# Kernel optimization log

Measured on AMD Instinct MI355X. Metric: run time of the kernel, lower is better.

Reference implementation:

```python
import jax, jax.numpy as jnp
import numpy as np

BIT_WIDTH = 1
LEVELS = 2 ** BIT_WIDTH - 1
# Floyd-Steinberg gather weights (mirrored scatter kernel): contributions to
# pixel (r,c) from (r-1,c-1), (r-1,c), (r-1,c+1), (r,c-1)
W_UL, W_U, W_UR, W_L = 1.0 / 16, 5.0 / 16, 3.0 / 16, 7.0 / 16


def quant(x):
    return jnp.round(x * LEVELS) / LEVELS


def dither(x01):
    """Raster-scan error-diffusion dithering. x01: [B,C,R,W] in [0,1]."""
    B, C, R, W = x01.shape
    dtype = x01.dtype

    def row_step(prev_err, row_x):
        # prev_err: [B,C,W+2] zero-padded errors of previous row
        # row_x:    [W,B,C]   input values of current row
        up = (W_UL * prev_err[..., 0:W]
              + W_U * prev_err[..., 1:W + 1]
              + W_UR * prev_err[..., 2:W + 2])          # [B,C,W]
        up = jnp.moveaxis(up, -1, 0)                     # [W,B,C]

        def col_step(left_err, xs):
            x, u = xs                                    # each [B,C]
            val = jnp.clip(x + u + W_L * left_err, 0.0, 1.0)
            err = val - quant(val)
            return err, (val, err)

        _, (vals, errs) = jax.lax.scan(col_step, jnp.zeros((B, C), dtype), (row_x, up))
        err_row = jnp.pad(jnp.moveaxis(errs, 0, -1), ((0, 0), (0, 0), (1, 1)))  # [B,C,W+2]
        return err_row, jnp.moveaxis(vals, 0, -1)        # carry, [B,C,W]

    rows_x = jnp.moveaxis(jnp.moveaxis(x01, 2, 0), -1, 1)  # [R,W,B,C]
    init = jnp.zeros((B, C, W + 2), dtype)
    _, out_rows = jax.lax.scan(row_step, init, rows_x)      # [R,B,C,W]
    out = jnp.moveaxis(out_rows, 0, 2)                      # [B,C,R,W]
    return quant(out)


def setup_inputs() -> dict:
    key = jax.random.key(0)
    x = jax.random.normal(key, (32, 3, 512, 512), dtype=jnp.float32)
    return {"x": x}


def reference(x):
    x = jnp.clip(x, -1.0, 1.0)
    x01 = (x + 1.0) / 2.0
    y = dither(x01)
    return y * 2.0 - 1.0
```

## Files before the change

### kernel.cpp

```cpp
#include <hip/hip_runtime.h>


#define F_UL 0.0625f
#define F_U  0.3125f
#define F_UR 0.1875f
#define F_L  0.4375f

constexpr int WW    = 512;
constexpr int IMG   = WW * WW;
constexpr int NIMG  = 96;
constexpr int NW    = 8;
constexpr int BUFW  = 792;
constexpr int NCH   = 40;
constexpr int LAG   = 10;
constexpr int PPAIR = 320;
constexpr size_t XP_FLOATS = (size_t)NIMG * NW * PPAIR * 128;
constexpr size_t XP_BYTES  = XP_FLOATS * 4;
constexpr size_t XP_SLACK  = 8192;
constexpr size_t XP_OFF    = 4u * 1024 * 1024;
constexpr size_t WS_NEED   = XP_OFF + XP_BYTES + XP_SLACK;

__device__ __forceinline__ float wave_shr1(float v, float fill) {
  int r = __builtin_amdgcn_update_dpp(__float_as_int(fill), __float_as_int(v),
                                      0x138 , 0xF, 0xF, false);
  return __int_as_float(r);
}

__device__ __forceinline__ float pp(float xv) {
#pragma clang fp contract(off)
  float xc = fminf(fmaxf(xv, -1.0f), 1.0f);
  return (xc + 1.0f) * 0.5f;
}

__global__ __launch_bounds__(256)
void pack_kernel(const float* __restrict__ xin, float* __restrict__ xp) {
  __shared__ float ring[4 * 4160];
  const int img = blockIdx.x, w = blockIdx.y;
  const int tid = threadIdx.x;
  const int wv  = tid >> 6, l = tid & 63;

  const float* xg = xin + (size_t)img * IMG + (size_t)w * 64 * WW;
  float* ob = xp + ((size_t)(img * NW + w) * PPAIR) * 128;

  auto load_tile = [&](int t) {
    float* dst = ring + (t & 3) * 4160;
    const float* src = xg + 64 * t;
#pragma unroll
    for (int k = 0; k < 4; ++k) {
      int flat = tid + 256 * k;
      int row = flat >> 4, cq = flat & 15;
      float4 v = *(const float4*)(src + row * WW + cq * 4);
      float* d = dst + row * 65 + cq * 4;
      d[0] = pp(v.x); d[1] = pp(v.y); d[2] = pp(v.z); d[3] = pp(v.w);
    }
  };

  load_tile(0);
  __syncthreads();
  for (int t = 0; t < 10; ++t) {
    if (t < 7) load_tile(t + 1);
    const int Mb = 32 * t + 8 * wv;
#pragma unroll
    for (int i = 0; i < 8; ++i) {
      const int M  = Mb + i;
      const int g  = 2 * (M - l);
      const int gm = g & 511;
      const int idx = ((gm >> 6) & 3) * 4160 + l * 65 + (gm & 63);
      const bool ok = ((unsigned)g < 512u);
      float va = ring[idx], vb = ring[idx + 1];
      float2 v = make_float2(ok ? va : -8.0f, ok ? vb : -8.0f);
      *(float2*)(ob + (size_t)M * 128 + 2 * l) = v;
    }
    __syncthreads();
  }
}

__global__ __launch_bounds__(512, 1)
void dither_packed(const float* __restrict__ xp, uint2* __restrict__ yb) {
  __shared__ float bnd[(NW + 1) * BUFW];
  __shared__ int flags[NW];

  const int  tid  = threadIdx.x;
  const int  wave = tid >> 6;
  const int  lane = tid & 63;
  const int  img  = blockIdx.x;
  const bool l63  = (lane == 63);

  for (int i = tid; i < (NW + 1) * BUFW; i += 512) bnd[i] = 0.0f;
  if (tid < NW) flags[tid] = 0;
  __syncthreads();

  uint2* ybw = yb + (size_t)(img * NW + wave) * (10 * 64);
  const float* xw = xp + ((size_t)(img * NW + wave) * PPAIR) * 128 + lane * 2;
  float* bufR = bnd + wave * BUFW;
  float* bufW = bnd + (wave + 1) * BUFW;

  float2 X0[4], X1[4], X2[4], X3[4], X4[4], X5[4], X6[4], X7[4];
#pragma unroll
  for (int i = 0; i < 4; ++i) {
    X0[i] = *(const float2*)(xw + (size_t)(0  + i) * 128);
    X1[i] = *(const float2*)(xw + (size_t)(4  + i) * 128);
    X2[i] = *(const float2*)(xw + (size_t)(8  + i) * 128);
    X3[i] = *(const float2*)(xw + (size_t)(12 + i) * 128);
  }

  int seen = 0;
  if (wave) {
    while ((seen = __hip_atomic_load(&flags[wave - 1], __ATOMIC_RELAXED,
                                     __HIP_MEMORY_SCOPE_WORKGROUP)) < LAG)
      __builtin_amdgcn_s_sleep(1);
    __asm__ volatile("s_waitcnt lgkmcnt(0)" ::: "memory");
  }

  float err = 0.0f, s2 = 0.0f;
  float s1 = (lane == 0) ? bufR[129] : 0.0f;
  float2 Q0[4], Q1[4];
#pragma unroll
  for (int i = 0; i < 4; ++i) {
    Q0[i] = *(const float2*)(bufR + 130 + 2 * i);
    Q1[i] = *(const float2*)(bufR + 138 + 2 * i);
  }

  unsigned accLo = 0u, accHi = 0u;

  auto step = [&](float qv, float xv) -> float {
#pragma clang fp contract(off)
    float e_in = wave_shr1(err, qv);
    float t1   = F_UL * s2;
    float t2   = F_U  * s1;
    float t3   = F_UR * e_in;
    float u    = (t1 + t2) + t3;
    float a1   = xv + u;
    float b    = F_L * err;
    float v    = a1 + b;
    float val  = __builtin_amdgcn_fmed3f(v, 0.0f, 1.0f);
    float qn   = rintf(val);
    err = val - qn;
    s2 = s1; s1 = e_in;
    return qn;
  };

  auto iter8 = [&](float2 (&XC)[4], float2 (&XL)[4], float2 (&QC)[4],
                   int T, int bsh, unsigned& acc) {
    const float* lp = xw + (size_t)(T / 2 + 16) * 128;
    XL[0] = *(const float2*)(lp + 0 * 128);
    XL[1] = *(const float2*)(lp + 1 * 128);
    XL[2] = *(const float2*)(lp + 2 * 128);
    XL[3] = *(const float2*)(lp + 3 * 128);

    float p0 = step(QC[0].x, XC[0].x); float e0 = err;
    float p1 = step(QC[0].y, XC[0].y); float e1 = err;
    float p2 = step(QC[1].x, XC[1].x); float e2 = err;
    float p3 = step(QC[1].y, XC[1].y); float e3 = err;
    float p4 = step(QC[2].x, XC[2].x); float e4 = err;
    float p5 = step(QC[2].y, XC[2].y); float e5 = err;
    float p6 = step(QC[3].x, XC[3].x); float e6 = err;
    float p7 = step(QC[3].y, XC[3].y); float e7 = err;

    QC[0] = *(const float2*)(bufR + (T + 146));
    QC[1] = *(const float2*)(bufR + (T + 148));
    QC[2] = *(const float2*)(bufR + (T + 150));
    QC[3] = *(const float2*)(bufR + (T + 152));

    acc |= ((__float_as_uint(p0) >> 29) & 1u) << (bsh + 0);
    acc |= ((__float_as_uint(p1) >> 29) & 1u) << (bsh + 1);
    acc |= ((__float_as_uint(p2) >> 29) & 1u) << (bsh + 2);
    acc |= ((__float_as_uint(p3) >> 29) & 1u) << (bsh + 3);
    acc |= ((__float_as_uint(p4) >> 29) & 1u) << (bsh + 4);
    acc |= ((__float_as_uint(p5) >> 29) & 1u) << (bsh + 5);
    acc |= ((__float_as_uint(p6) >> 29) & 1u) << (bsh + 6);
    acc |= ((__float_as_uint(p7) >> 29) & 1u) << (bsh + 7);

    if (l63) {
      float* bw = bufW + (T + 3);
      bw[0] = e0; bw[1] = e1; bw[2] = e2; bw[3] = e3;
      bw[4] = e4; bw[5] = e5; bw[6] = e6; bw[7] = e7;
    }
  };

  auto waitflag = [&](int j) {
    if (wave) {
      int need = j + LAG; if (need > NCH) need = NCH;
      if (seen < need) {
        while ((seen = __hip_atomic_load(&flags[wave - 1], __ATOMIC_RELAXED,
                                         __HIP_MEMORY_SCOPE_WORKGROUP)) < need)
          __builtin_amdgcn_s_sleep(1);
        __asm__ volatile("s_waitcnt lgkmcnt(0)" ::: "memory");
      }
    }
  };
  auto pubflag = [&](int v) {
    if (l63) {
      __asm__ volatile("s_waitcnt lgkmcnt(0)" ::: "memory");
      __hip_atomic_store(&flags[wave], v, __ATOMIC_RELAXED,
                         __HIP_MEMORY_SCOPE_WORKGROUP);
    }
  };

  for (int jj = 0; jj < NCH; jj += 4) {
    const int T0 = 16 * jj;
    waitflag(jj);
    iter8(X0, X4, Q0, T0 + 0,  0,  accLo);
    iter8(X1, X5, Q1, T0 + 8,  8,  accLo);
    pubflag(jj + 1);
    waitflag(jj + 1);
    iter8(X2, X6, Q0, T0 + 16, 16, accLo);
    iter8(X3, X7, Q1, T0 + 24, 24, accLo);
    pubflag(jj + 2);
    waitflag(jj + 2);
    iter8(X4, X0, Q0, T0 + 32, 0,  accHi);
    iter8(X5, X1, Q1, T0 + 40, 8,  accHi);
    pubflag(jj + 3);
    waitflag(jj + 3);
    iter8(X6, X2, Q0, T0 + 48, 16, accHi);
    iter8(X7, X3, Q1, T0 + 56, 24, accHi);
    pubflag(jj + 4);
    ybw[(jj >> 2) * 64 + lane] = make_uint2(accLo, accHi);
    accLo = 0u; accHi = 0u;
  }
}

__global__ __launch_bounds__(256)
void unpack_kernel(const unsigned long long* __restrict__ yb,
                   float* __restrict__ yout) {
  const int img = blockIdx.x, w = blockIdx.y;
  const int wv = threadIdx.x >> 6, lane = threadIdx.x & 63;
  const unsigned long long* ybr = yb + (size_t)(img * NW + w) * 640;
  float* yb0 = yout + (size_t)img * IMG + (size_t)w * 64 * WW;

  for (int rr = 0; rr < 16; ++rr) {
    const int r  = wv * 16 + rr;
    const int t0 = 8 * lane + 2 * r;
    const int t64 = t0 >> 6, sh = t0 & 63;
    unsigned long long w1 = ybr[(size_t)t64 * 64 + r];
    unsigned long long w2 = ybr[(size_t)(t64 + 1) * 64 + r];
    unsigned bits = (unsigned)((w1 >> sh) | ((w2 << 1) << (63 - sh)));
    float* orow = yb0 + (size_t)r * WW + 8 * lane;
    float4 v0, v1;
    v0.x = (bits & 1u)   ? 1.0f : -1.0f;
    v0.y = (bits & 2u)   ? 1.0f : -1.0f;
    v0.z = (bits & 4u)   ? 1.0f : -1.0f;
    v0.w = (bits & 8u)   ? 1.0f : -1.0f;
    v1.x = (bits & 16u)  ? 1.0f : -1.0f;
    v1.y = (bits & 32u)  ? 1.0f : -1.0f;
    v1.z = (bits & 64u)  ? 1.0f : -1.0f;
    v1.w = (bits & 128u) ? 1.0f : -1.0f;
    *(float4*)(orow)     = v0;
    *(float4*)(orow + 4) = v1;
  }
}

__global__ __launch_bounds__(512, 1)
void dither_direct(const float* __restrict__ xin, float* __restrict__ yout) {
  __shared__ float bnd[(NW + 1) * BUFW];
  __shared__ int flags[NW];

  const int  tid  = threadIdx.x;
  const int  wave = tid >> 6;
  const int  lane = tid & 63;
  const int  img  = blockIdx.x;
  const bool l63  = (lane == 63);

  for (int i = tid; i < (NW + 1) * BUFW; i += 512) bnd[i] = 0.0f;
  if (tid < NW) flags[tid] = 0;
  __syncthreads();

  const int r = wave * 64 + lane;
  const float* xrow = xin + (size_t)img * IMG + (size_t)r * WW;
  float*       yrow = yout + (size_t)img * IMG + (size_t)r * WW;
  float* bufR = bnd + wave * BUFW;
  float* bufW = bnd + (wave + 1) * BUFW;
  const int c0 = -2 * lane;

  auto ldx = [&](int c) -> float2 { return *(const float2*)(xrow + (c & 511)); };

  float2 A0 = ldx(c0 + 0),  A1 = ldx(c0 + 2),  A2 = ldx(c0 + 4),  A3 = ldx(c0 + 6);
  float2 pB0 = ldx(c0 + 8),  pB1 = ldx(c0 + 10), pB2 = ldx(c0 + 12), pB3 = ldx(c0 + 14);
  float2 pC0 = ldx(c0 + 16), pC1 = ldx(c0 + 18), pC2 = ldx(c0 + 20), pC3 = ldx(c0 + 22);
  float xq0 = pp(A0.x), xq1 = pp(A0.y), xq2 = pp(A1.x), xq3 = pp(A1.y);
  float xq4 = pp(A2.x), xq5 = pp(A2.y), xq6 = pp(A3.x), xq7 = pp(A3.y);
  float2 pA0 = pB0, pA1 = pB1, pA2 = pB2, pA3 = pB3;
  pB0 = pC0; pB1 = pC1; pB2 = pC2; pB3 = pC3;

  if (wave) {
    while (__hip_atomic_load(&flags[wave - 1], __ATOMIC_RELAXED,
                             __HIP_MEMORY_SCOPE_WORKGROUP) < LAG)
      __builtin_amdgcn_s_sleep(1);
    __asm__ volatile("s_waitcnt lgkmcnt(0)" ::: "memory");
  }

  float err = 0.0f, s2 = 0.0f;
  float s1 = (lane == 0) ? bufR[129] : 0.0f;
  float2 qa = *(const float2*)(bufR + 130);
  float2 qb = *(const float2*)(bufR + 132);
  float2 qc = *(const float2*)(bufR + 134);
  float2 qd = *(const float2*)(bufR + 136);
  float2 fa = *(const float2*)(bufR + 138);
  float2 fb = *(const float2*)(bufR + 140);
  float2 fc = *(const float2*)(bufR + 142);
  float2 fd = *(const float2*)(bufR + 144);

  auto step = [&](int c, float qv, float xv) -> float {
#pragma clang fp contract(off)
    float e_in = wave_shr1(err, qv);
    float t1   = F_UL * s2;
    float t2   = F_U  * s1;
    float t3   = F_UR * e_in;
    float u    = (t1 + t2) + t3;
    float a1   = xv + u;
    float b    = F_L * err;
    float v    = a1 + b;
    float val  = fminf(fmaxf(v, 0.0f), 1.0f);
    float qn   = rintf(val);
    float e    = val - qn;
    float en   = ((unsigned)c < 512u) ? e : 0.0f;
    err = en; s2 = s1; s1 = e_in;
    return __builtin_fmaf(qn, 2.0f, -1.0f);
  };

  auto iter8 = [&](int T) {
    const int cg = c0 + T;
    float2 n0 = ldx(cg + 24), n1 = ldx(cg + 26), n2 = ldx(cg + 28), n3 = ldx(cg + 30);
    float2 h0 = *(const float2*)(bufR + (T + 146));
    float2 h1 = *(const float2*)(bufR + (T + 148));
    float2 h2 = *(const float2*)(bufR + (T + 150));
    float2 h3 = *(const float2*)(bufR + (T + 152));
    float w0 = pp(pA0.x), w1 = pp(pA0.y), w2 = pp(pA1.x), w3 = pp(pA1.y);
    float w4 = pp(pA2.x), w5 = pp(pA2.y), w6 = pp(pA3.x), w7 = pp(pA3.y);

    float y0 = step(cg + 0, qa.x, xq0); float e0 = err;
    float y1 = step(cg + 1, qa.y, xq1); float e1 = err;
    float y2 = step(cg + 2, qb.x, xq2); float e2 = err;
    float y3 = step(cg + 3, qb.y, xq3); float e3 = err;
    float y4 = step(cg + 4, qc.x, xq4); float e4 = err;
    float y5 = step(cg + 5, qc.y, xq5); float e5 = err;
    float y6 = step(cg + 6, qd.x, xq6); float e6 = err;
    float y7 = step(cg + 7, qd.y, xq7); float e7 = err;

    if ((unsigned)(cg + 0) < 511u) *(float2*)(yrow + cg + 0) = make_float2(y0, y1);
    if ((unsigned)(cg + 2) < 511u) *(float2*)(yrow + cg + 2) = make_float2(y2, y3);
    if ((unsigned)(cg + 4) < 511u) *(float2*)(yrow + cg + 4) = make_float2(y4, y5);
    if ((unsigned)(cg + 6) < 511u) *(float2*)(yrow + cg + 6) = make_float2(y6, y7);

    if (l63) {
      float* bw = bufW + (cg + 129);
      bw[0] = e0; bw[1] = e1; bw[2] = e2; bw[3] = e3;
      bw[4] = e4; bw[5] = e5; bw[6] = e6; bw[7] = e7;
    }

    xq0 = w0; xq1 = w1; xq2 = w2; xq3 = w3;
    xq4 = w4; xq5 = w5; xq6 = w6; xq7 = w7;
    pA0 = pB0; pA1 = pB1; pA2 = pB2; pA3 = pB3;
    pB0 = n0;  pB1 = n1;  pB2 = n2;  pB3 = n3;
    qa = fa; qb = fb; qc = fc; qd = fd;
    fa = h0; fb = h1; fc = h2; fd = h3;
  };

  for (int j = 0; j < NCH; ++j) {
    if (wave) {
      int need = j + LAG; if (need > NCH) need = NCH;
      while (__hip_atomic_load(&flags[wave - 1], __ATOMIC_RELAXED,
                               __HIP_MEMORY_SCOPE_WORKGROUP) < need)
        __builtin_amdgcn_s_sleep(1);
      __asm__ volatile("s_waitcnt lgkmcnt(0)" ::: "memory");
    }
    iter8(16 * j);
    iter8(16 * j + 8);
    if (l63) {
      __asm__ volatile("s_waitcnt lgkmcnt(0)" ::: "memory");
      __hip_atomic_store(&flags[wave], j + 1, __ATOMIC_RELAXED,
                         __HIP_MEMORY_SCOPE_WORKGROUP);
    }
  }
}

extern "C" void kernel_launch(void* const* d_in, const int* in_sizes, int n_in,
                              void* d_out, int out_size, void* d_ws, size_t ws_size,
                              hipStream_t stream) {
  const float* x = (const float*)d_in[0];
  float*       y = (float*)d_out;
  if (ws_size >= WS_NEED) {
    unsigned long long* yb = (unsigned long long*)d_ws;
    float* xp = (float*)((char*)d_ws + XP_OFF);
    pack_kernel<<<dim3(NIMG, NW), dim3(256), 0, stream>>>(x, xp);
    dither_packed<<<dim3(NIMG), dim3(512), 0, stream>>>(xp, (uint2*)yb);
    unpack_kernel<<<dim3(NIMG, NW), dim3(256), 0, stream>>>(yb, y);
  } else {
    dither_direct<<<dim3(NIMG), dim3(512), 0, stream>>>(x, y);
  }
}
```

Measured before the change: 282.6 us.

## Fuse pack, dither and unpack into one kernel with global flag handoff

Merges the three launches into one grid. The first NIMG*NW blocks pack input tiles, then each publishes a per-(image, wave) global flag with release semantics. The remaining NIMG blocks spin on those flags, run the dither, keep the result bits in shared memory and expand them straight to the output. This removes two kernel launches and the global round trip of the bit buffer, and lets dithering of early images overlap packing of later ones. It adds a memset, spin-waits that rely on packer blocks being scheduled before the dither blocks, and heavier per-block shared memory that may limit co-residency.

```diff
diff --git a/kernel.cpp b/kernel.cpp
--- a/kernel.cpp
+++ b/kernel.cpp
@@ -5,6 +5,8 @@
 #define F_U  0.3125f
 #define F_UR 0.1875f
 #define F_L  0.4375f
+
+typedef unsigned long long ull;
 
 constexpr int WW    = 512;
 constexpr int IMG   = WW * WW;
@@ -14,11 +16,21 @@
 constexpr int NCH   = 40;
 constexpr int LAG   = 10;
 constexpr int PPAIR = 320;
+constexpr int NPACK = NIMG * NW;
+constexpr int GRID  = NPACK + NIMG;
+
 constexpr size_t XP_FLOATS = (size_t)NIMG * NW * PPAIR * 128;
 constexpr size_t XP_BYTES  = XP_FLOATS * 4;
 constexpr size_t XP_SLACK  = 8192;
 constexpr size_t XP_OFF    = 4u * 1024 * 1024;
 constexpr size_t WS_NEED   = XP_OFF + XP_BYTES + XP_SLACK;
+constexpr size_t FLAGS_BYTES = (size_t)NPACK * 4;
+
+constexpr int BND_BYTES  = (NW + 1) * BUFW * 4;
+constexpr int FLAGS_OFF  = BND_BYTES;
+constexpr int BITS_OFF   = BND_BYTES + 32;
+constexpr int BITS_BYTES = NW * 11 * 64 * 8;
+constexpr int SMEM_BYTES = BITS_OFF + BITS_BYTES;
 
 __device__ __forceinline__ float wave_shr1(float v, float fill) {
   int r = __builtin_amdgcn_update_dpp(__float_as_int(fill), __float_as_int(v),
@@ -32,65 +44,81 @@
   return (xc + 1.0f) * 0.5f;
 }
 
-__global__ __launch_bounds__(256)
-void pack_kernel(const float* __restrict__ xin, float* __restrict__ xp) {
-  __shared__ float ring[4 * 4160];
-  const int img = blockIdx.x, w = blockIdx.y;
+__global__ __launch_bounds__(512, 1)
+void fused(const float* __restrict__ xin, float* __restrict__ xp,
+           int* __restrict__ gflags, float* __restrict__ yout) {
+  __shared__ alignas(16) unsigned char smem[SMEM_BYTES];
+  const int bid = blockIdx.x;
   const int tid = threadIdx.x;
-  const int wv  = tid >> 6, l = tid & 63;
-
-  const float* xg = xin + (size_t)img * IMG + (size_t)w * 64 * WW;
-  float* ob = xp + ((size_t)(img * NW + w) * PPAIR) * 128;
-
-  auto load_tile = [&](int t) {
-    float* dst = ring + (t & 3) * 4160;
-    const float* src = xg + 64 * t;
+
+  if (bid < NPACK) {
+    const int w   = bid / NIMG;
+    const int img = bid % NIMG;
+    const int wv  = tid >> 6, l = tid & 63;
+    float* ring = (float*)smem;
+
+    const float* xg = xin + (size_t)img * IMG + (size_t)w * 64 * WW;
+    float* ob = xp + ((size_t)(img * NW + w) * PPAIR) * 128;
+
+    auto load_tile = [&](int t) {
+      float* dst = ring + (t & 3) * 4160;
+      const float* src = xg + 64 * t;
 #pragma unroll
-    for (int k = 0; k < 4; ++k) {
-      int flat = tid + 256 * k;
-      int row = flat >> 4, cq = flat & 15;
-      float4 v = *(const float4*)(src + row * WW + cq * 4);
-      float* d = dst + row * 65 + cq * 4;
-      d[0] = pp(v.x); d[1] = pp(v.y); d[2] = pp(v.z); d[3] = pp(v.w);
-    }
-  };
-
-  load_tile(0);
-  __syncthreads();
-  for (int t = 0; t < 10; ++t) {
-    if (t < 7) load_tile(t + 1);
-    const int Mb = 32 * t + 8 * wv;
+      for (int k = 0; k < 2; ++k) {
+        int flat = tid + 512 * k;
+        int row = flat >> 4, cq = flat & 15;
+        float4 v = *(const float4*)(src + row * WW + cq * 4);
+        float* d = dst + row * 65 + cq * 4;
+        d[0] = pp(v.x); d[1] = pp(v.y); d[2] = pp(v.z); d[3] = pp(v.w);
+      }
+    };
+
+    load_tile(0);
+    __syncthreads();
+    for (int t = 0; t < 10; ++t) {
+      if (t < 7) load_tile(t + 1);
+      const int Mb = 32 * t + 4 * wv;
 #pragma unroll
-    for (int i = 0; i < 8; ++i) {
-      const int M  = Mb + i;
-      const int g  = 2 * (M - l);
-      const int gm = g & 511;
-      const int idx = ((gm >> 6) & 3) * 4160 + l * 65 + (gm & 63);
-      const bool ok = ((unsigned)g < 512u);
-      float va = ring[idx], vb = ring[idx + 1];
-      float2 v = make_float2(ok ? va : -8.0f, ok ? vb : -8.0f);
-      *(float2*)(ob + (size_t)M * 128 + 2 * l) = v;
-    }
-    __syncthreads();
-  }
-}
-
-__global__ __launch_bounds__(512, 1)
-void dither_packed(const float* __restrict__ xp, uint2* __restrict__ yb) {
-  __shared__ float bnd[(NW + 1) * BUFW];
-  __shared__ int flags[NW];
-
-  const int  tid  = threadIdx.x;
+      for (int i = 0; i < 4; ++i) {
+        const int M  = Mb + i;
+        const int g  = 2 * (M - l);
+        const int gm = g & 511;
+        const int idx = ((gm >> 6) & 3) * 4160 + l * 65 + (gm & 63);
+        const bool ok = ((unsigned)g < 512u);
+        float va = ring[idx], vb = ring[idx + 1];
+        float2 v = make_float2(ok ? va : -8.0f, ok ? vb : -8.0f);
+        *(float2*)(ob + (size_t)M * 128 + 2 * l) = v;
+      }
+      __syncthreads();
+    }
+    __threadfence();
+    if (tid == 0)
+      __hip_atomic_store(&gflags[img * NW + w], 1, __ATOMIC_RELEASE,
+                         __HIP_MEMORY_SCOPE_AGENT);
+    return;
+  }
+
+  const int  img  = bid - NPACK;
   const int  wave = tid >> 6;
   const int  lane = tid & 63;
-  const int  img  = blockIdx.x;
   const bool l63  = (lane == 63);
+
+  float* bnd  = (float*)smem;
+  int*   flags = (int*)(smem + FLAGS_OFF);
+  ull (*bits)[11][64] = (ull (*)[11][64])(smem + BITS_OFF);
 
   for (int i = tid; i < (NW + 1) * BUFW; i += 512) bnd[i] = 0.0f;
   if (tid < NW) flags[tid] = 0;
+  bits[wave][10][lane] = 0ull;
   __syncthreads();
 
-  uint2* ybw = yb + (size_t)(img * NW + wave) * (10 * 64);
+  {
+    const int* gf = gflags + img * NW + wave;
+    while (__hip_atomic_load(gf, __ATOMIC_ACQUIRE,
+                             __HIP_MEMORY_SCOPE_AGENT) == 0)
+      __builtin_amdgcn_s_sleep(16);
+  }
+
   const float* xw = xp + ((size_t)(img * NW + wave) * PPAIR) * 128 + lane * 2;
   float* bufR = bnd + wave * BUFW;
   float* bufW = bnd + (wave + 1) * BUFW;
@@ -215,36 +243,27 @@
     iter8(X6, X2, Q0, T0 + 48, 16, accHi);
     iter8(X7, X3, Q1, T0 + 56, 24, accHi);
     pubflag(jj + 4);
-    ybw[(jj >> 2) * 64 + lane] = make_uint2(accLo, accHi);
+    *(uint2*)&bits[wave][jj >> 2][lane] = make_uint2(accLo, accHi);
     accLo = 0u; accHi = 0u;
   }
-}
-
-__global__ __launch_bounds__(256)
-void unpack_kernel(const unsigned long long* __restrict__ yb,
-                   float* __restrict__ yout) {
-  const int img = blockIdx.x, w = blockIdx.y;
-  const int wv = threadIdx.x >> 6, lane = threadIdx.x & 63;
-  const unsigned long long* ybr = yb + (size_t)(img * NW + w) * 640;
-  float* yb0 = yout + (size_t)img * IMG + (size_t)w * 64 * WW;
-
-  for (int rr = 0; rr < 16; ++rr) {
-    const int r  = wv * 16 + rr;
+
+  float* ybase = yout + (size_t)img * IMG + (size_t)(wave * 64) * WW + 8 * lane;
+  for (int r = 0; r < 64; ++r) {
     const int t0 = 8 * lane + 2 * r;
     const int t64 = t0 >> 6, sh = t0 & 63;
-    unsigned long long w1 = ybr[(size_t)t64 * 64 + r];
-    unsigned long long w2 = ybr[(size_t)(t64 + 1) * 64 + r];
-    unsigned bits = (unsigned)((w1 >> sh) | ((w2 << 1) << (63 - sh)));
-    float* orow = yb0 + (size_t)r * WW + 8 * lane;
+    ull w1 = bits[wave][t64][r];
+    ull w2 = bits[wave][t64 + 1][r];
+    unsigned b = (unsigned)((w1 >> sh) | ((w2 << 1) << (63 - sh)));
+    float* orow = ybase + (size_t)r * WW;
     float4 v0, v1;
-    v0.x = (bits & 1u)   ? 1.0f : -1.0f;
-    v0.y = (bits & 2u)   ? 1.0f : -1.0f;
-    v0.z = (bits & 4u)   ? 1.0f : -1.0f;
-    v0.w = (bits & 8u)   ? 1.0f : -1.0f;
-    v1.x = (bits & 16u)  ? 1.0f : -1.0f;
-    v1.y = (bits & 32u)  ? 1.0f : -1.0f;
-    v1.z = (bits & 64u)  ? 1.0f : -1.0f;
-    v1.w = (bits & 128u) ? 1.0f : -1.0f;
+    v0.x = (b & 1u)   ? 1.0f : -1.0f;
+    v0.y = (b & 2u)   ? 1.0f : -1.0f;
+    v0.z = (b & 4u)   ? 1.0f : -1.0f;
+    v0.w = (b & 8u)   ? 1.0f : -1.0f;
+    v1.x = (b & 16u)  ? 1.0f : -1.0f;
+    v1.y = (b & 32u)  ? 1.0f : -1.0f;
+    v1.z = (b & 64u)  ? 1.0f : -1.0f;
+    v1.w = (b & 128u) ? 1.0f : -1.0f;
     *(float4*)(orow)     = v0;
     *(float4*)(orow + 4) = v1;
   }
@@ -380,11 +399,10 @@
   const float* x = (const float*)d_in[0];
   float*       y = (float*)d_out;
   if (ws_size >= WS_NEED) {
-    unsigned long long* yb = (unsigned long long*)d_ws;
-    float* xp = (float*)((char*)d_ws + XP_OFF);
-    pack_kernel<<<dim3(NIMG, NW), dim3(256), 0, stream>>>(x, xp);
-    dither_packed<<<dim3(NIMG), dim3(512), 0, stream>>>(xp, (uint2*)yb);
-    unpack_kernel<<<dim3(NIMG, NW), dim3(256), 0, stream>>>(yb, y);
+    int*   gflags = (int*)d_ws;
+    float* xp     = (float*)((char*)d_ws + XP_OFF);
+    hipMemsetAsync(d_ws, 0, FLAGS_BYTES, stream);
+    fused<<<dim3(GRID), dim3(512), 0, stream>>>(x, xp, gflags, y);
   } else {
     dither_direct<<<dim3(NIMG), dim3(512), 0, stream>>>(x, y);
   }
```

New measurement: 505.2 us. 78.8% more time.

## Fuse unpack into dither kernel and run two strips per wave

Applied to the files above, without the earlier changes.

The separate unpack kernel is removed. Packed result bits now stay in shared memory and each block expands them to ±1 floats at the end. The dither kernel drops from 8 to 4 waves per block, each wave handling two 64-row strips in sequence with the same flag-based wavefront pipeline, so each SIMD holds one wave instead of two. This removes a launch and the global round trip for the bit buffer. The cost is that the output writes happen at the tail of only 96 blocks instead of being spread over a wide grid, and shared memory use grows.

```diff
diff --git a/kernel.cpp b/kernel.cpp
--- a/kernel.cpp
+++ b/kernel.cpp
@@ -5,6 +5,8 @@
 #define F_U  0.3125f
 #define F_UR 0.1875f
 #define F_L  0.4375f
+
+typedef unsigned long long ull;
 
 constexpr int WW    = 512;
 constexpr int IMG   = WW * WW;
@@ -75,10 +77,11 @@
   }
 }
 
-__global__ __launch_bounds__(512, 1)
-void dither_packed(const float* __restrict__ xp, uint2* __restrict__ yb) {
+__global__ __launch_bounds__(256, 1)
+void dither_packed4(const float* __restrict__ xp, float* __restrict__ yout) {
   __shared__ float bnd[(NW + 1) * BUFW];
-  __shared__ int flags[NW];
+  __shared__ int   flags[NW];
+  __shared__ ull   bits[NW][11][65];
 
   const int  tid  = threadIdx.x;
   const int  wave = tid >> 6;
@@ -86,167 +89,166 @@
   const int  img  = blockIdx.x;
   const bool l63  = (lane == 63);
 
-  for (int i = tid; i < (NW + 1) * BUFW; i += 512) bnd[i] = 0.0f;
+  for (int i = tid; i < (NW + 1) * BUFW; i += 256) bnd[i] = 0.0f;
   if (tid < NW) flags[tid] = 0;
+  bits[wave][10][lane] = 0ull;
+  bits[wave + 4][10][lane] = 0ull;
   __syncthreads();
 
-  uint2* ybw = yb + (size_t)(img * NW + wave) * (10 * 64);
-  const float* xw = xp + ((size_t)(img * NW + wave) * PPAIR) * 128 + lane * 2;
-  float* bufR = bnd + wave * BUFW;
-  float* bufW = bnd + (wave + 1) * BUFW;
-
-  float2 X0[4], X1[4], X2[4], X3[4], X4[4], X5[4], X6[4], X7[4];
+  for (int half = 0; half < 2; ++half) {
+    const int p = wave + 4 * half;
+    const float* xw = xp + ((size_t)(img * NW + p) * PPAIR) * 128 + lane * 2;
+    float* bufR = bnd + p * BUFW;
+    float* bufW = bnd + (p + 1) * BUFW;
+    ull*   bitp = &bits[p][0][0];
+
+    float2 X0[4], X1[4], X2[4], X3[4], X4[4], X5[4], X6[4], X7[4];
 #pragma unroll
-  for (int i = 0; i < 4; ++i) {
-    X0[i] = *(const float2*)(xw + (size_t)(0  + i) * 128);
-    X1[i] = *(const float2*)(xw + (size_t)(4  + i) * 128);
-    X2[i] = *(const float2*)(xw + (size_t)(8  + i) * 128);
-    X3[i] = *(const float2*)(xw + (size_t)(12 + i) * 128);
-  }
-
-  int seen = 0;
-  if (wave) {
-    while ((seen = __hip_atomic_load(&flags[wave - 1], __ATOMIC_RELAXED,
-                                     __HIP_MEMORY_SCOPE_WORKGROUP)) < LAG)
-      __builtin_amdgcn_s_sleep(1);
-    __asm__ volatile("s_waitcnt lgkmcnt(0)" ::: "memory");
-  }
-
-  float err = 0.0f, s2 = 0.0f;
-  float s1 = (lane == 0) ? bufR[129] : 0.0f;
-  float2 Q0[4], Q1[4];
+    for (int i = 0; i < 4; ++i) {
+      X0[i] = *(const float2*)(xw + (size_t)(0  + i) * 128);
+      X1[i] = *(const float2*)(xw + (size_t)(4  + i) * 128);
+      X2[i] = *(const float2*)(xw + (size_t)(8  + i) * 128);
+      X3[i] = *(const float2*)(xw + (size_t)(12 + i) * 128);
+    }
+
+    int seen = 0;
+    if (p) {
+      while ((seen = __hip_atomic_load(&flags[p - 1], __ATOMIC_RELAXED,
+                                       __HIP_MEMORY_SCOPE_WORKGROUP)) < LAG)
+        __builtin_amdgcn_s_sleep(1);
+      __asm__ volatile("s_waitcnt lgkmcnt(0)" ::: "memory");
+    }
+
+    float err = 0.0f, s2 = 0.0f;
+    float s1 = (lane == 0) ? bufR[129] : 0.0f;
+    float2 Q0[4], Q1[4];
 #pragma unroll
-  for (int i = 0; i < 4; ++i) {
-    Q0[i] = *(const float2*)(bufR + 130 + 2 * i);
-    Q1[i] = *(const float2*)(bufR + 138 + 2 * i);
-  }
-
-  unsigned accLo = 0u, accHi = 0u;
-
-  auto step = [&](float qv, float xv) -> float {
+    for (int i = 0; i < 4; ++i) {
+      Q0[i] = *(const float2*)(bufR + 130 + 2 * i);
+      Q1[i] = *(const float2*)(bufR + 138 + 2 * i);
+    }
+
+    unsigned accLo = 0u, accHi = 0u;
+
+    auto step = [&](float qv, float xv) -> float {
 #pragma clang fp contract(off)
-    float e_in = wave_shr1(err, qv);
-    float t1   = F_UL * s2;
-    float t2   = F_U  * s1;
-    float t3   = F_UR * e_in;
-    float u    = (t1 + t2) + t3;
-    float a1   = xv + u;
-    float b    = F_L * err;
-    float v    = a1 + b;
-    float val  = __builtin_amdgcn_fmed3f(v, 0.0f, 1.0f);
-    float qn   = rintf(val);
-    err = val - qn;
-    s2 = s1; s1 = e_in;
-    return qn;
-  };
-
-  auto iter8 = [&](float2 (&XC)[4], float2 (&XL)[4], float2 (&QC)[4],
-                   int T, int bsh, unsigned& acc) {
-    const float* lp = xw + (size_t)(T / 2 + 16) * 128;
-    XL[0] = *(const float2*)(lp + 0 * 128);
-    XL[1] = *(const float2*)(lp + 1 * 128);
-    XL[2] = *(const float2*)(lp + 2 * 128);
-    XL[3] = *(const float2*)(lp + 3 * 128);
-
-    float p0 = step(QC[0].x, XC[0].x); float e0 = err;
-    float p1 = step(QC[0].y, XC[0].y); float e1 = err;
-    float p2 = step(QC[1].x, XC[1].x); float e2 = err;
-    float p3 = step(QC[1].y, XC[1].y); float e3 = err;
-    float p4 = step(QC[2].x, XC[2].x); float e4 = err;
-    float p5 = step(QC[2].y, XC[2].y); float e5 = err;
-    float p6 = step(QC[3].x, XC[3].x); float e6 = err;
-    float p7 = step(QC[3].y, XC[3].y); float e7 = err;
-
-    QC[0] = *(const float2*)(bufR + (T + 146));
-    QC[1] = *(const float2*)(bufR + (T + 148));
-    QC[2] = *(const float2*)(bufR + (T + 150));
-    QC[3] = *(const float2*)(bufR + (T + 152));
-
-    acc |= ((__float_as_uint(p0) >> 29) & 1u) << (bsh + 0);
-    acc |= ((__float_as_uint(p1) >> 29) & 1u) << (bsh + 1);
-    acc |= ((__float_as_uint(p2) >> 29) & 1u) << (bsh + 2);
-    acc |= ((__float_as_uint(p3) >> 29) & 1u) << (bsh + 3);
-    acc |= ((__float_as_uint(p4) >> 29) & 1u) << (bsh + 4);
-    acc |= ((__float_as_uint(p5) >> 29) & 1u) << (bsh + 5);
-    acc |= ((__float_as_uint(p6) >> 29) & 1u) << (bsh + 6);
-    acc |= ((__float_as_uint(p7) >> 29) & 1u) << (bsh + 7);
-
-    if (l63) {
-      float* bw = bufW + (T + 3);
-      bw[0] = e0; bw[1] = e1; bw[2] = e2; bw[3] = e3;
-      bw[4] = e4; bw[5] = e5; bw[6] = e6; bw[7] = e7;
-    }
-  };
-
-  auto waitflag = [&](int j) {
-    if (wave) {
-      int need = j + LAG; if (need > NCH) need = NCH;
-      if (seen < need) {
-        while ((seen = __hip_atomic_load(&flags[wave - 1], __ATOMIC_RELAXED,
-                                         __HIP_MEMORY_SCOPE_WORKGROUP)) < need)
-          __builtin_amdgcn_s_sleep(1);
+      float e_in = wave_shr1(err, qv);
+      float t1   = F_UL * s2;
+      float t2   = F_U  * s1;
+      float t3   = F_UR * e_in;
+      float u    = (t1 + t2) + t3;
+      float a1   = xv + u;
+      float b    = F_L * err;
+      float v    = a1 + b;
+      float val  = __builtin_amdgcn_fmed3f(v, 0.0f, 1.0f);
+      float qn   = rintf(val);
+      err = val - qn;
+      s2 = s1; s1 = e_in;
+      return qn;
+    };
+
+    auto iter8 = [&](float2 (&XC)[4], float2 (&XL)[4], float2 (&QC)[4],
+                     int T, int bsh, unsigned& acc) {
+      const float* lp = xw + (size_t)(T / 2 + 16) * 128;
+      XL[0] = *(const float2*)(lp + 0 * 128);
+      XL[1] = *(const float2*)(lp + 1 * 128);
+      XL[2] = *(const float2*)(lp + 2 * 128);
+      XL[3] = *(const float2*)(lp + 3 * 128);
+
+      float p0 = step(QC[0].x, XC[0].x); float e0 = err;
+      float p1 = step(QC[0].y, XC[0].y); float e1 = err;
+      float p2 = step(QC[1].x, XC[1].x); float e2 = err;
+      float p3 = step(QC[1].y, XC[1].y); float e3 = err;
+      float p4 = step(QC[2].x, XC[2].x); float e4 = err;
+      float p5 = step(QC[2].y, XC[2].y); float e5 = err;
+      float p6 = step(QC[3].x, XC[3].x); float e6 = err;
+      float p7 = step(QC[3].y, XC[3].y); float e7 = err;
+
+      QC[0] = *(const float2*)(bufR + (T + 146));
+      QC[1] = *(const float2*)(bufR + (T + 148));
+      QC[2] = *(const float2*)(bufR + (T + 150));
+      QC[3] = *(const float2*)(bufR + (T + 152));
+
+      acc |= ((__float_as_uint(p0) >> 29) & 1u) << (bsh + 0);
+      acc |= ((__float_as_uint(p1) >> 29) & 1u) << (bsh + 1);
+      acc |= ((__float_as_uint(p2) >> 29) & 1u) << (bsh + 2);
+      acc |= ((__float_as_uint(p3) >> 29) & 1u) << (bsh + 3);
+      acc |= ((__float_as_uint(p4) >> 29) & 1u) << (bsh + 4);
+      acc |= ((__float_as_uint(p5) >> 29) & 1u) << (bsh + 5);
+      acc |= ((__float_as_uint(p6) >> 29) & 1u) << (bsh + 6);
+      acc |= ((__float_as_uint(p7) >> 29) & 1u) << (bsh + 7);
+
+      if (l63) {
+        float* bw = bufW + (T + 3);
+        bw[0] = e0; bw[1] = e1; bw[2] = e2; bw[3] = e3;
+        bw[4] = e4; bw[5] = e5; bw[6] = e6; bw[7] = e7;
+      }
+    };
+
+    auto waitflag = [&](int j) {
+      if (p) {
+        int need = j + LAG; if (need > NCH) need = NCH;
+        if (seen < need) {
+          while ((seen = __hip_atomic_load(&flags[p - 1], __ATOMIC_RELAXED,
+                                           __HIP_MEMORY_SCOPE_WORKGROUP)) < need)
+            __builtin_amdgcn_s_sleep(1);
+          __asm__ volatile("s_waitcnt lgkmcnt(0)" ::: "memory");
+        }
+      }
+    };
+    auto pubflag = [&](int v) {
+      if (l63) {
         __asm__ volatile("s_waitcnt lgkmcnt(0)" ::: "memory");
+        __hip_atomic_store(&flags[p], v, __ATOMIC_RELAXED,
+                           __HIP_MEMORY_SCOPE_WORKGROUP);
       }
-    }
-  };
-  auto pubflag = [&](int v) {
-    if (l63) {
-      __asm__ volatile("s_waitcnt lgkmcnt(0)" ::: "memory");
-      __hip_atomic_store(&flags[wave], v, __ATOMIC_RELAXED,
-                         __HIP_MEMORY_SCOPE_WORKGROUP);
-    }
-  };
-
-  for (int jj = 0; jj < NCH; jj += 4) {
-    const int T0 = 16 * jj;
-    waitflag(jj);
-    iter8(X0, X4, Q0, T0 + 0,  0,  accLo);
-    iter8(X1, X5, Q1, T0 + 8,  8,  accLo);
-    pubflag(jj + 1);
-    waitflag(jj + 1);
-    iter8(X2, X6, Q0, T0 + 16, 16, accLo);
-    iter8(X3, X7, Q1, T0 + 24, 24, accLo);
-    pubflag(jj + 2);
-    waitflag(jj + 2);
-    iter8(X4, X0, Q0, T0 + 32, 0,  accHi);
-    iter8(X5, X1, Q1, T0 + 40, 8,  accHi);
-    pubflag(jj + 3);
-    waitflag(jj + 3);
-    iter8(X6, X2, Q0, T0 + 48, 16, accHi);
-    iter8(X7, X3, Q1, T0 + 56, 24, accHi);
-    pubflag(jj + 4);
-    ybw[(jj >> 2) * 64 + lane] = make_uint2(accLo, accHi);
-    accLo = 0u; accHi = 0u;
-  }
-}
-
-__global__ __launch_bounds__(256)
-void unpack_kernel(const unsigned long long* __restrict__ yb,
-                   float* __restrict__ yout) {
-  const int img = blockIdx.x, w = blockIdx.y;
-  const int wv = threadIdx.x >> 6, lane = threadIdx.x & 63;
-  const unsigned long long* ybr = yb + (size_t)(img * NW + w) * 640;
-  float* yb0 = yout + (size_t)img * IMG + (size_t)w * 64 * WW;
-
-  for (int rr = 0; rr < 16; ++rr) {
-    const int r  = wv * 16 + rr;
-    const int t0 = 8 * lane + 2 * r;
-    const int t64 = t0 >> 6, sh = t0 & 63;
-    unsigned long long w1 = ybr[(size_t)t64 * 64 + r];
-    unsigned long long w2 = ybr[(size_t)(t64 + 1) * 64 + r];
-    unsigned bits = (unsigned)((w1 >> sh) | ((w2 << 1) << (63 - sh)));
-    float* orow = yb0 + (size_t)r * WW + 8 * lane;
-    float4 v0, v1;
-    v0.x = (bits & 1u)   ? 1.0f : -1.0f;
-    v0.y = (bits & 2u)   ? 1.0f : -1.0f;
-    v0.z = (bits & 4u)   ? 1.0f : -1.0f;
-    v0.w = (bits & 8u)   ? 1.0f : -1.0f;
-    v1.x = (bits & 16u)  ? 1.0f : -1.0f;
-    v1.y = (bits & 32u)  ? 1.0f : -1.0f;
-    v1.z = (bits & 64u)  ? 1.0f : -1.0f;
-    v1.w = (bits & 128u) ? 1.0f : -1.0f;
-    *(float4*)(orow)     = v0;
-    *(float4*)(orow + 4) = v1;
+    };
+
+    for (int jj = 0; jj < NCH; jj += 4) {
+      const int T0 = 16 * jj;
+      waitflag(jj);
+      iter8(X0, X4, Q0, T0 + 0,  0,  accLo);
+      iter8(X1, X5, Q1, T0 + 8,  8,  accLo);
+      pubflag(jj + 1);
+      waitflag(jj + 1);
+      iter8(X2, X6, Q0, T0 + 16, 16, accLo);
+      iter8(X3, X7, Q1, T0 + 24, 24, accLo);
+      pubflag(jj + 2);
+      waitflag(jj + 2);
+      iter8(X4, X0, Q0, T0 + 32, 0,  accHi);
+      iter8(X5, X1, Q1, T0 + 40, 8,  accHi);
+      pubflag(jj + 3);
+      waitflag(jj + 3);
+      iter8(X6, X2, Q0, T0 + 48, 16, accHi);
+      iter8(X7, X3, Q1, T0 + 56, 24, accHi);
+      pubflag(jj + 4);
+      *(uint2*)(bitp + (size_t)(jj >> 2) * 65 + lane) = make_uint2(accLo, accHi);
+      accLo = 0u; accHi = 0u;
+    }
+  }
+
+  for (int half = 0; half < 2; ++half) {
+    const int p = wave + 4 * half;
+    float* ybase = yout + (size_t)img * IMG + (size_t)(p * 64) * WW + 8 * lane;
+    for (int rr = 0; rr < 64; ++rr) {
+      const int t0 = 8 * lane + 2 * rr;
+      const int t64 = t0 >> 6, sh = t0 & 63;
+      ull w1 = bits[p][t64][rr];
+      ull w2 = bits[p][t64 + 1][rr];
+      unsigned b = (unsigned)((w1 >> sh) | ((w2 << 1) << (63 - sh)));
+      float* orow = ybase + (size_t)rr * WW;
+      float4 v0, v1;
+      v0.x = (b & 1u)   ? 1.0f : -1.0f;
+      v0.y = (b & 2u)   ? 1.0f : -1.0f;
+      v0.z = (b & 4u)   ? 1.0f : -1.0f;
+      v0.w = (b & 8u)   ? 1.0f : -1.0f;
+      v1.x = (b & 16u)  ? 1.0f : -1.0f;
+      v1.y = (b & 32u)  ? 1.0f : -1.0f;
+      v1.z = (b & 64u)  ? 1.0f : -1.0f;
+      v1.w = (b & 128u) ? 1.0f : -1.0f;
+      *(float4*)(orow)     = v0;
+      *(float4*)(orow + 4) = v1;
+    }
   }
 }
 
@@ -380,11 +382,9 @@
   const float* x = (const float*)d_in[0];
   float*       y = (float*)d_out;
   if (ws_size >= WS_NEED) {
-    unsigned long long* yb = (unsigned long long*)d_ws;
     float* xp = (float*)((char*)d_ws + XP_OFF);
     pack_kernel<<<dim3(NIMG, NW), dim3(256), 0, stream>>>(x, xp);
-    dither_packed<<<dim3(NIMG), dim3(512), 0, stream>>>(xp, (uint2*)yb);
-    unpack_kernel<<<dim3(NIMG, NW), dim3(256), 0, stream>>>(yb, y);
+    dither_packed4<<<dim3(NIMG), dim3(256), 0, stream>>>(xp, y);
   } else {
     dither_direct<<<dim3(NIMG), dim3(512), 0, stream>>>(x, y);
   }
```

New measurement: 282.7 us. About the same (+0.0%).
